# Kernel tuning notes

Hardware: AMD Instinct MI355X
Metric: run time of the kernel (lower is better)

The kernel has to match this reference:

```python
import jax, jax.numpy as jnp
import numpy as np

B, N, T = 64, 256, 512          # batch, num_objs, num_triples
DO, DP, H, DOUT = 512, 512, 512, 512


def setup_inputs() -> dict:
    key = jax.random.key(0)
    ks = jax.random.split(key, 12)

    def kaiming(k, shape):
        fan_in = shape[0]
        return jax.random.normal(k, shape, jnp.float32) * np.sqrt(2.0 / fan_in)

    return {
        "obj_vecs": jax.random.normal(ks[0], (B, N, DO), jnp.float32),
        "pred_vecs": jax.random.normal(ks[1], (B, T, DP), jnp.float32),
        "edges": jax.random.randint(ks[2], (B, T, 3), 0, N, jnp.int64),
        # net1: [2*DO+DP -> H -> 2*H+DOUT], ReLU after each Linear
        "n1_w1": kaiming(ks[3], (2 * DO + DP, H)),
        "n1_b1": jnp.zeros((H,), jnp.float32),
        "n1_w2": kaiming(ks[4], (H, 2 * H + DOUT)),
        "n1_b2": jnp.zeros((2 * H + DOUT,), jnp.float32),
        # net2: [H -> H -> DOUT], ReLU after each Linear
        "n2_w1": kaiming(ks[5], (H, H)),
        "n2_b1": jnp.zeros((H,), jnp.float32),
        "n2_w2": kaiming(ks[6], (H, DOUT)),
        "n2_b2": jnp.zeros((DOUT,), jnp.float32),
    }


def reference(obj_vecs, pred_vecs, edges,
              n1_w1, n1_b1, n1_w2, n1_b2,
              n2_w1, n2_b1, n2_w2, n2_b2):
    num_batch, num_objs, _ = obj_vecs.shape
    h_dim = n1_b1.shape[0]
    d_out = n2_w2.shape[1]

    s_idx = edges[:, :, 0]            # [B, T] subject node ids
    o_idx = edges[:, :, 2]            # [B, T] object node ids

    # gather subject/object vectors per triple
    cur_s = jnp.take_along_axis(obj_vecs, s_idx[:, :, None], axis=1)  # [B,T,DO]
    cur_o = jnp.take_along_axis(obj_vecs, o_idx[:, :, None], axis=1)  # [B,T,DO]
    cur_t = jnp.concatenate([cur_s, pred_vecs, cur_o], axis=-1)       # [B,T,2DO+DP]

    # net1 MLP (Linear+ReLU, Linear+ReLU)
    hid = jax.nn.relu(jnp.einsum('btd,dh->bth', cur_t, n1_w1) + n1_b1)
    new_t = jax.nn.relu(jnp.einsum('bth,hk->btk', hid, n1_w2) + n1_b2)

    new_s = new_t[:, :, :h_dim]
    new_p = new_t[:, :, h_dim:h_dim + d_out]
    new_o = new_t[:, :, h_dim + d_out:2 * h_dim + d_out]

    # scatter-add back to nodes, per batch element
    b_ix = jnp.arange(num_batch)[:, None]            # [B,1]
    pooled = jnp.zeros((num_batch, num_objs, h_dim), obj_vecs.dtype)
    pooled = pooled.at[b_ix, s_idx].add(new_s)
    pooled = pooled.at[b_ix, o_idx].add(new_o)

    # avg pooling: divide by per-node incidence count (clamped at 1)
    ones = jnp.ones(s_idx.shape, obj_vecs.dtype)
    counts = jnp.zeros((num_batch, num_objs), obj_vecs.dtype)
    counts = counts.at[b_ix, s_idx].add(ones)
    counts = counts.at[b_ix, o_idx].add(ones)
    counts = jnp.maximum(counts, 1.0)
    pooled = pooled / counts[:, :, None]

    # net2 MLP (Linear+ReLU, Linear+ReLU)
    h2 = jax.nn.relu(jnp.einsum('bnh,hk->bnk', pooled, n2_w1) + n2_b1)
    new_obj_vecs = jax.nn.relu(jnp.einsum('bnh,hd->bnd', h2, n2_w2) + n2_b2)

    return new_obj_vecs, new_p
```

## Files before the change

### kernel.cpp

```cpp
#include <hip/hip_runtime.h>

typedef __bf16 bf16;
typedef __attribute__((ext_vector_type(2))) __bf16 bf16x2;
typedef __attribute__((ext_vector_type(4))) __bf16 bf16x4;
typedef __attribute__((ext_vector_type(8))) __bf16 bf16x8;
typedef __attribute__((ext_vector_type(4))) float f32x4;

#define DEVINL __device__ __forceinline__

typedef __attribute__((address_space(1))) void gvoid_t;
typedef __attribute__((address_space(3))) void lvoid_t;

DEVINL void async_ld16(const void* g, void* l) {
    __builtin_amdgcn_global_load_lds((gvoid_t*)g, (lvoid_t*)l, 16, 0, 0);
}

template<int MODE, int NBN>
__global__ __launch_bounds__(256, 2) void gemm_k(
    const bf16* __restrict__ A, const bf16* __restrict__ Bt,
    const float* __restrict__ bias, bf16* __restrict__ Dbf,
    float* __restrict__ Df, bf16* __restrict__ Dbf2,
    const int* __restrict__ edges, const bf16* __restrict__ obj,
    const bf16* __restrict__ pred, int K)
{
    const int tid = threadIdx.x;
    const int id = blockIdx.x;
    const int bn = (id >> 3) % NBN;
    const int bm = (id & 7) + 8 * ((id >> 3) / NBN);

    __shared__ __align__(16) bf16 lds[2 * 128 * 64];
    bf16* ldsA = lds;
    bf16* ldsB = lds + 128 * 64;

    const int g_slot = tid & 7;
    const int row0 = tid >> 3;

    unsigned offS[4], offP[4], offO[4], offA[4], offB[4];
#pragma unroll
    for (int i = 0; i < 4; i++) {
        int r = row0 + 32 * i;
        int gr = bm * 128 + r;
        if (MODE == 0) {
            int b = gr >> 9;
            int s = edges[gr * 3 + 0] & 255;
            int o = edges[gr * 3 + 2] & 255;
            offS[i] = (unsigned)(b * 256 + s) * 512u;
            offP[i] = (unsigned)gr * 512u;
            offO[i] = (unsigned)(b * 256 + o) * 512u;
        } else {
            offA[i] = (unsigned)gr * (unsigned)K;
        }
        offB[i] = (unsigned)(bn * 128 + r) * (unsigned)K;
    }

    f32x4 acc[4][4];
    const f32x4 zero4 = {0.f, 0.f, 0.f, 0.f};
#pragma unroll
    for (int i = 0; i < 4; i++)
#pragma unroll
        for (int j = 0; j < 4; j++) acc[i][j] = zero4;

    const int wave = tid >> 6;
    const int lane = tid & 63;
    const int wr = (wave >> 1) * 64;
    const int wc = (wave & 1) * 64;
    const int lq = lane >> 4;
    const int lr = lane & 15;

    const int KT = K >> 6;
    for (int kt = 0; kt < KT; ++kt) {
        __syncthreads();
#pragma unroll
        for (int i = 0; i < 4; i++) {
            int r = row0 + 32 * i;
            int gsrc = g_slot ^ (r & 7);
            const bf16* gp;
            if (MODE == 0) {
                int region = kt >> 3;
                unsigned col = (unsigned)((kt & 7) * 64 + gsrc * 8);
                if (region == 0)      gp = obj + offS[i] + col;
                else if (region == 1) gp = pred + offP[i] + col;
                else                  gp = obj + offO[i] + col;
            } else {
                gp = A + offA[i] + (unsigned)(kt * 64 + gsrc * 8);
            }
            async_ld16(gp, ldsA + (tid + i * 256) * 8);
        }
#pragma unroll
        for (int i = 0; i < 4; i++) {
            int r = row0 + 32 * i;
            int gsrc = g_slot ^ (r & 7);
            async_ld16(Bt + offB[i] + (unsigned)(kt * 64 + gsrc * 8),
                       ldsB + (tid + i * 256) * 8);
        }
        __syncthreads();

#pragma unroll
        for (int ks = 0; ks < 2; ++ks) {
            bf16x8 af[4], bfr[4];
#pragma unroll
            for (int mi = 0; mi < 4; ++mi) {
                int r = wr + mi * 16 + lr;
                int g = (ks * 4 + lq) ^ (r & 7);
                af[mi] = *(const bf16x8*)(ldsA + (r * 8 + g) * 8);
            }
#pragma unroll
            for (int ni = 0; ni < 4; ++ni) {
                int r = wc + ni * 16 + lr;
                int g = (ks * 4 + lq) ^ (r & 7);
                bfr[ni] = *(const bf16x8*)(ldsB + (r * 8 + g) * 8);
            }
#pragma unroll
            for (int mi = 0; mi < 4; ++mi)
#pragma unroll
                for (int ni = 0; ni < 4; ++ni)
                    acc[mi][ni] = __builtin_amdgcn_mfma_f32_16x16x32_bf16(
                        bfr[ni], af[mi], acc[mi][ni], 0, 0, 0);
        }
    }

    __syncthreads();

    const int rb = bm * 128 + wr;
    const bool f32path = (MODE == 3) || (MODE == 1 && bn >= 4 && bn < 8);

    if (!f32path) {
        bf16* cw = lds + wave * 4096;
        const bf16*  dummy = nullptr; (void)dummy;
        bf16* outp;
        int cb;
        if (MODE == 1) {
            if (bn < 4) { outp = Dbf;  cb = bn * 128 + wc; }
            else        { outp = Dbf2; cb = bn * 128 + wc - 1024; }
        } else {
            outp = Dbf; cb = bn * 128 + wc;
        }
#pragma unroll
        for (int ni = 0; ni < 4; ++ni) {
            const f32x4 bv = *(const f32x4*)(bias + bn * 128 + wc + ni * 16 + lq * 4);
#pragma unroll
            for (int mi = 0; mi < 4; ++mi) {
                f32x4 v = acc[mi][ni];
                int row = mi * 16 + lr;
                int sl = (ni * 2 + (lq >> 1)) ^ (row & 7);
                bf16x4 o4;
#pragma unroll
                for (int r = 0; r < 4; r++) {
                    float t = v[r] + bv[r];
                    o4[r] = (bf16)(t > 0.f ? t : 0.f);
                }
                *(bf16x4*)(cw + row * 64 + sl * 8 + (lq & 1) * 4) = o4;
            }
        }
#pragma unroll
        for (int it = 0; it < 8; ++it) {
            int g = it * 64 + lane;
            int row = g >> 3, k = g & 7;
            bf16x8 v = *(const bf16x8*)(cw + row * 64 + ((k ^ (row & 7)) * 8));
            *(bf16x8*)(outp + (unsigned)(rb + row) * 512u + cb + k * 8) = v;
        }
    } else {
        float* cwf = (float*)lds + wave * 2048;
        const int cbf = (MODE == 1) ? (bn * 128 + wc - 512) : (bn * 128 + wc);
#pragma unroll
        for (int half = 0; half < 2; ++half) {
#pragma unroll
            for (int ni = 0; ni < 4; ++ni) {
                const f32x4 bv = *(const f32x4*)(bias + bn * 128 + wc + ni * 16 + lq * 4);
#pragma unroll
                for (int mi2 = 0; mi2 < 2; ++mi2) {
                    f32x4 v = acc[half * 2 + mi2][ni];
                    int row = mi2 * 16 + lr;
                    int s16 = ni * 4 + lq;
                    int sl = (s16 & 8) | ((s16 & 7) ^ (row & 7));
                    f32x4 x;
#pragma unroll
                    for (int r = 0; r < 4; r++) {
                        float t = v[r] + bv[r];
                        x[r] = t > 0.f ? t : 0.f;
                    }
                    *(f32x4*)(cwf + row * 64 + sl * 4) = x;
                }
            }
#pragma unroll
            for (int it = 0; it < 8; ++it) {
                int g = it * 64 + lane;
                int row = g >> 4, k = g & 15;
                int kk = (k & 8) | ((k & 7) ^ (row & 7));
                f32x4 v = *(const f32x4*)(cwf + row * 64 + kk * 4);
                *(f32x4*)(Df + (unsigned)(rb + half * 32 + row) * 512u + cbf + k * 4) = v;
            }
        }
    }
}

__global__ void pre_k(const float4* __restrict__ o, const float4* __restrict__ p,
                      bf16x4* __restrict__ ob, bf16x4* __restrict__ pb,
                      const float* __restrict__ w1, bf16* __restrict__ w1t,
                      const float* __restrict__ w2, bf16* __restrict__ w2t,
                      const float* __restrict__ w3, bf16* __restrict__ w3t,
                      const float* __restrict__ w4, bf16* __restrict__ w4t) {
    __shared__ float tile[32][33];
    int blk = blockIdx.x;
    int t = threadIdx.x;
    if (blk >= 24576) {
        int id = blk - 24576;
        const float* src; bf16* dst; int R, C, bx, by;
        if (id < 768)       { src = w1; dst = w1t; R = 1536; C = 512;  bx = id % 16; by = id / 16; }
        else if (id < 1536) { id -= 768;  src = w2; dst = w2t; R = 512; C = 1536; bx = id % 48; by = id / 48; }
        else if (id < 1792) { id -= 1536; src = w3; dst = w3t; R = 512; C = 512;  bx = id % 16; by = id / 16; }
        else                { id -= 1792; src = w4; dst = w4t; R = 512; C = 512;  bx = id % 16; by = id / 16; }
        int c0 = bx * 32, r0 = by * 32;
        int tx = t & 31, ty = t >> 5;
#pragma unroll
        for (int i = 0; i < 4; i++)
            tile[ty + i * 8][tx] = src[(size_t)(r0 + ty + i * 8) * C + c0 + tx];
        __syncthreads();
#pragma unroll
        for (int i = 0; i < 4; i++)
            dst[(size_t)(c0 + ty + i * 8) * R + r0 + tx] = (bf16)tile[tx][ty + i * 8];
        return;
    }
    int i = blk * 256 + t;
    if (i < 2097152) {
        float4 v = o[i];
        bf16x4 r = { (bf16)v.x, (bf16)v.y, (bf16)v.z, (bf16)v.w };
        ob[i] = r;
    } else {
        int j = i - 2097152;
        float4 v = p[j];
        bf16x4 r = { (bf16)v.x, (bf16)v.y, (bf16)v.z, (bf16)v.w };
        pb[j] = r;
    }
}

__global__ __launch_bounds__(256) void pool3_k(
    const int* __restrict__ edges,
    const bf16* __restrict__ new_s, const bf16* __restrict__ new_o,
    bf16* __restrict__ out)
{
    __shared__ int ent[1024];
    __shared__ int ec;
    const int idx = blockIdx.x;
    const int b = idx >> 8, n = idx & 255;
    const int t = threadIdx.x;
    if (t == 0) ec = 0;
    __syncthreads();
#pragma unroll
    for (int e0 = 0; e0 < 2; e0++) {
        int row = b * 512 + t + e0 * 256;
        int s = edges[row * 3 + 0] & 255;
        int o = edges[row * 3 + 2] & 255;
        if (s == n) { int ps = atomicAdd(&ec, 1); ent[ps] = row << 1; }
        if (o == n) { int po = atomicAdd(&ec, 1); ent[po] = (row << 1) | 1; }
    }
    __syncthreads();
    const int c = ec;
    float a0 = 0.f, a1 = 0.f;
    for (int j = 0; j < c; ++j) {
        int v = ent[j];
        const bf16x2* rp = (const bf16x2*)(((v & 1) ? new_o : new_s) +
                                           (unsigned)(v >> 1) * 512u);
        bf16x2 w = rp[t];
        a0 += (float)w[0];
        a1 += (float)w[1];
    }
    float inv = 1.f / (float)(c > 1 ? c : 1);
    bf16x2 o2 = { (bf16)(a0 * inv), (bf16)(a1 * inv) };
    *(bf16x2*)(out + (unsigned)idx * 512u + (unsigned)(t * 2)) = o2;
}

extern "C" void kernel_launch(void* const* d_in, const int* in_sizes, int n_in,
                              void* d_out, int out_size, void* d_ws, size_t ws_size,
                              hipStream_t stream) {
    const float* obj_f  = (const float*)d_in[0];
    const float* pred_f = (const float*)d_in[1];
    const int*   edges  = (const int*)d_in[2];
    const float* w1 = (const float*)d_in[3];
    const float* b1 = (const float*)d_in[4];
    const float* w2 = (const float*)d_in[5];
    const float* b2 = (const float*)d_in[6];
    const float* w3 = (const float*)d_in[7];
    const float* b3 = (const float*)d_in[8];
    const float* w4 = (const float*)d_in[9];
    const float* b4 = (const float*)d_in[10];

    char* ws = (char*)d_ws;
    bf16* obj_bf  = (bf16*)(ws + 0);
    bf16* pred_bf = (bf16*)(ws + 16777216);
    bf16* new_s   = (bf16*)(ws + 0);
    bf16* w1t = (bf16*)(ws + 50331648);
    bf16* w2t = (bf16*)(ws + 51904512);
    bf16* w3t = (bf16*)(ws + 53477376);
    bf16* w4t = (bf16*)(ws + 54001664);
    bf16* hid = (bf16*)(ws + 54525952);
    bf16* pooled_bf = hid;
    bf16* h2  = (bf16*)(ws + 71303168);

    float* out_obj = (float*)d_out;
    float* out_p   = (float*)d_out + 8388608;
    bf16* new_o    = (bf16*)d_out;

    pre_k<<<26624, 256, 0, stream>>>((const float4*)obj_f, (const float4*)pred_f,
                                     (bf16x4*)obj_bf, (bf16x4*)pred_bf,
                                     w1, w1t, w2, w2t, w3, w3t, w4, w4t);

    gemm_k<0, 4><<<1024, 256, 0, stream>>>(
        nullptr, w1t, b1, hid, nullptr, nullptr, edges, obj_bf, pred_bf, 1536);

    gemm_k<1, 12><<<3072, 256, 0, stream>>>(
        hid, w2t, b2, new_s, out_p, new_o, nullptr, nullptr, nullptr, 512);

    pool3_k<<<16384, 256, 0, stream>>>(edges, new_s, new_o, pooled_bf);

    gemm_k<2, 4><<<512, 256, 0, stream>>>(
        pooled_bf, w3t, b3, h2, nullptr, nullptr, nullptr, nullptr, nullptr, 512);

    gemm_k<3, 4><<<512, 256, 0, stream>>>(
        h2, w4t, b4, nullptr, out_obj, nullptr, nullptr, nullptr, nullptr, 512);
}
```

Measured before the change: 367.0 us.

## Use 256x256-tile 8-wave pipelined GEMM kernel for net1 layers

Adds a new 512-thread GEMM kernel with 256x256 output tiles, double-buffered LDS staging in quarter chunks, and explicit vmcnt/lgkmcnt waits so global-to-LDS loads and register fragment loads overlap MFMA work. The two large net1 GEMMs (gather-fused first layer and the wide second layer) move to it, while net2 keeps the old 128x128 kernel, now trimmed to its two modes. The larger tiles raise arithmetic intensity and cut redundant operand loads. In exchange they use 128 KB of LDS, many accumulator registers and fewer blocks, which could limit occupancy and tail balance.

```diff
diff --git a/kernel.cpp b/kernel.cpp
--- a/kernel.cpp
+++ b/kernel.cpp
@@ -15,41 +15,250 @@
     __builtin_amdgcn_global_load_lds((gvoid_t*)g, (lvoid_t*)l, 16, 0, 0);
 }
 
-template<int MODE, int NBN>
-__global__ __launch_bounds__(256, 2) void gemm_k(
+DEVINL void wait_vm6()   { asm volatile("s_waitcnt vmcnt(6)" ::: "memory"); }
+DEVINL void wait_vm4()   { asm volatile("s_waitcnt vmcnt(4)" ::: "memory"); }
+DEVINL void wait_vm0()   { asm volatile("s_waitcnt vmcnt(0)" ::: "memory"); }
+DEVINL void wait_lgkm0() { asm volatile("s_waitcnt lgkmcnt(0)" ::: "memory");
+                           __builtin_amdgcn_sched_barrier(0); }
+DEVINL void barrier_()   { __builtin_amdgcn_s_barrier();
+                           __builtin_amdgcn_sched_barrier(0); }
+
+template<int MODE>
+__global__ __launch_bounds__(512, 2) void gemm8_k(
     const bf16* __restrict__ A, const bf16* __restrict__ Bt,
     const float* __restrict__ bias, bf16* __restrict__ Dbf,
     float* __restrict__ Df, bf16* __restrict__ Dbf2,
     const int* __restrict__ edges, const bf16* __restrict__ obj,
-    const bf16* __restrict__ pred, int K)
+    const bf16* __restrict__ pred, int K, int NBN)
 {
     const int tid = threadIdx.x;
     const int id = blockIdx.x;
     const int bn = (id >> 3) % NBN;
     const int bm = (id & 7) + 8 * ((id >> 3) / NBN);
 
-    __shared__ __align__(16) bf16 lds[2 * 128 * 64];
-    bf16* ldsA = lds;
-    bf16* ldsB = lds + 128 * 64;
+    __shared__ __align__(16) bf16 lds[8 * 8192];
 
     const int g_slot = tid & 7;
     const int row0 = tid >> 3;
 
     unsigned offS[4], offP[4], offO[4], offA[4], offB[4];
 #pragma unroll
-    for (int i = 0; i < 4; i++) {
-        int r = row0 + 32 * i;
-        int gr = bm * 128 + r;
+    for (int hi = 0; hi < 4; hi++) {
+        int r = (hi >> 1) * 128 + (hi & 1) * 64 + row0;
+        int gr = bm * 256 + r;
         if (MODE == 0) {
             int b = gr >> 9;
             int s = edges[gr * 3 + 0] & 255;
             int o = edges[gr * 3 + 2] & 255;
-            offS[i] = (unsigned)(b * 256 + s) * 512u;
-            offP[i] = (unsigned)gr * 512u;
-            offO[i] = (unsigned)(b * 256 + o) * 512u;
+            offS[hi] = (unsigned)(b * 256 + s) * 512u;
+            offP[hi] = (unsigned)gr * 512u;
+            offO[hi] = (unsigned)(b * 256 + o) * 512u;
         } else {
-            offA[i] = (unsigned)gr * (unsigned)K;
-        }
+            offA[hi] = (unsigned)gr * (unsigned)K;
+        }
+        offB[hi] = (unsigned)(bn * 256 + r) * (unsigned)K;
+    }
+
+    auto STAGE = [&](int tt, int kind) {
+        bf16* ldst = lds + ((tt & 1) * 4 + kind) * 8192;
+        int h = kind & 1;
+#pragma unroll
+        for (int i = 0; i < 2; i++) {
+            int r = i * 64 + row0;
+            int gsrc = g_slot ^ (r & 7);
+            int hi = h * 2 + i;
+            const bf16* gp;
+            if (kind < 2) {
+                if (MODE == 0) {
+                    int region = tt >> 3;
+                    unsigned col = (unsigned)((tt & 7) * 64 + gsrc * 8);
+                    if (region == 0)      gp = obj + offS[hi] + col;
+                    else if (region == 1) gp = pred + offP[hi] + col;
+                    else                  gp = obj + offO[hi] + col;
+                } else {
+                    gp = A + offA[hi] + (unsigned)(tt * 64 + gsrc * 8);
+                }
+            } else {
+                gp = Bt + offB[hi] + (unsigned)(tt * 64 + gsrc * 8);
+            }
+            async_ld16(gp, ldst + (tid + i * 512) * 8);
+        }
+    };
+
+    f32x4 acc[8][4];
+    const f32x4 zero4 = {0.f, 0.f, 0.f, 0.f};
+#pragma unroll
+    for (int i = 0; i < 8; i++)
+#pragma unroll
+        for (int j = 0; j < 4; j++) acc[i][j] = zero4;
+
+    const int wave = tid >> 6, lane = tid & 63;
+    const int wm = wave >> 2, wn = wave & 3;
+    const int lq = lane >> 4, lr = lane & 15;
+
+    bf16x8 af0[8], af1[8], b0r[4], b1r[4];
+
+    auto LDA = [&](int tt, int ks, bf16x8* d) {
+        const bf16* base = lds + ((tt & 1) * 4 + wm) * 8192;
+#pragma unroll
+        for (int mi = 0; mi < 8; mi++) {
+            int rr = mi * 16 + lr;
+            int g = (ks * 4 + lq) ^ (rr & 7);
+            d[mi] = *(const bf16x8*)(base + (rr * 8 + g) * 8);
+        }
+    };
+    auto LDB = [&](int tt, int ks, bf16x8* d) {
+        const bf16* base = lds + ((tt & 1) * 4 + 2 + (wn >> 1)) * 8192;
+#pragma unroll
+        for (int ni = 0; ni < 4; ni++) {
+            int rr = (wn & 1) * 64 + ni * 16 + lr;
+            int g = (ks * 4 + lq) ^ (rr & 7);
+            d[ni] = *(const bf16x8*)(base + (rr * 8 + g) * 8);
+        }
+    };
+    auto MM = [&](const bf16x8* a, const bf16x8* b, int mh) {
+        __builtin_amdgcn_s_setprio(1);
+#pragma unroll
+        for (int mi = 0; mi < 4; mi++)
+#pragma unroll
+            for (int ni = 0; ni < 4; ni++)
+                acc[mh * 4 + mi][ni] = __builtin_amdgcn_mfma_f32_16x16x32_bf16(
+                    b[ni], a[mh * 4 + mi], acc[mh * 4 + mi][ni], 0, 0, 0);
+        __builtin_amdgcn_s_setprio(0);
+        __builtin_amdgcn_sched_barrier(0);
+    };
+
+    STAGE(0, 0); STAGE(0, 1); STAGE(0, 2); STAGE(0, 3);
+
+    const int NT = K >> 6;
+    for (int t = 0; ; ++t) {
+        if (t < NT) {
+            if (t + 1 < NT) { STAGE(t + 1, 0); wait_vm6(); }
+            else            wait_vm4();
+        } else wait_vm0();
+        barrier_();
+        if (t < NT) LDA(t, 0, af0);
+        wait_lgkm0();
+        if (t >= 1) MM(af1, b1r, 0);
+        barrier_();
+        if (t < NT) {
+            if (t + 1 < NT) { STAGE(t + 1, 1); wait_vm4(); }
+            else            wait_vm0();
+        }
+        barrier_();
+        if (t < NT) LDB(t, 0, b0r);
+        wait_lgkm0();
+        if (t >= 1) MM(af1, b1r, 1);
+        barrier_();
+        if (t == NT) break;
+        if (t + 1 < NT) STAGE(t + 1, 2);
+        barrier_();
+        LDA(t, 1, af1);
+        wait_lgkm0();
+        MM(af0, b0r, 0);
+        barrier_();
+        if (t + 1 < NT) STAGE(t + 1, 3);
+        barrier_();
+        LDB(t, 1, b1r);
+        wait_lgkm0();
+        MM(af0, b0r, 1);
+        barrier_();
+    }
+
+    const int rowbase = bm * 256 + wm * 128;
+    const int cb0 = bn * 256 + wn * 64;
+    const bool f32p = (MODE == 1) && (cb0 >= 512) && (cb0 < 1024);
+
+    if (!f32p) {
+        bf16* cw = lds + wave * 8192;
+        bf16* outp; int cb;
+        if (MODE == 1) {
+            if (cb0 < 512) { outp = Dbf;  cb = cb0; }
+            else           { outp = Dbf2; cb = cb0 - 1024; }
+        } else { outp = Dbf; cb = cb0; }
+#pragma unroll
+        for (int ni = 0; ni < 4; ++ni) {
+            const f32x4 bv = *(const f32x4*)(bias + cb0 + ni * 16 + lq * 4);
+#pragma unroll
+            for (int mi = 0; mi < 8; ++mi) {
+                f32x4 v = acc[mi][ni];
+                int row = mi * 16 + lr;
+                int sl = (ni * 2 + (lq >> 1)) ^ (row & 7);
+                bf16x4 o4;
+#pragma unroll
+                for (int r = 0; r < 4; r++) {
+                    float x = v[r] + bv[r];
+                    o4[r] = (bf16)(x > 0.f ? x : 0.f);
+                }
+                *(bf16x4*)(cw + row * 64 + sl * 8 + (lq & 1) * 4) = o4;
+            }
+        }
+#pragma unroll
+        for (int it = 0; it < 16; ++it) {
+            int g = it * 64 + lane;
+            int row = g >> 3, k = g & 7;
+            bf16x8 v = *(const bf16x8*)(cw + row * 64 + ((k ^ (row & 7)) * 8));
+            *(bf16x8*)(outp + (unsigned)(rowbase + row) * 512u + cb + k * 8) = v;
+        }
+    } else {
+        float* cwf = (float*)lds + wave * 4096;
+        const int cbf = cb0 - 512;
+#pragma unroll
+        for (int mh = 0; mh < 2; ++mh) {
+#pragma unroll
+            for (int ni = 0; ni < 4; ++ni) {
+                const f32x4 bv = *(const f32x4*)(bias + cb0 + ni * 16 + lq * 4);
+#pragma unroll
+                for (int mi2 = 0; mi2 < 4; ++mi2) {
+                    f32x4 v = acc[mh * 4 + mi2][ni];
+                    int row = mi2 * 16 + lr;
+                    int s16 = ni * 4 + lq;
+                    int sl = (s16 & 8) | ((s16 & 7) ^ (row & 7));
+                    f32x4 x;
+#pragma unroll
+                    for (int r = 0; r < 4; r++) {
+                        float tt = v[r] + bv[r];
+                        x[r] = tt > 0.f ? tt : 0.f;
+                    }
+                    *(f32x4*)(cwf + row * 64 + sl * 4) = x;
+                }
+            }
+#pragma unroll
+            for (int it = 0; it < 16; ++it) {
+                int g = it * 64 + lane;
+                int row = g >> 4, k = g & 15;
+                int kk = (k & 8) | ((k & 7) ^ (row & 7));
+                f32x4 v = *(const f32x4*)(cwf + row * 64 + kk * 4);
+                *(f32x4*)(Df + (unsigned)(rowbase + mh * 64 + row) * 512u
+                          + cbf + k * 4) = v;
+            }
+        }
+    }
+}
+
+template<int MODE, int NBN>
+__global__ __launch_bounds__(256, 2) void gemm_k(
+    const bf16* __restrict__ A, const bf16* __restrict__ Bt,
+    const float* __restrict__ bias, bf16* __restrict__ Dbf,
+    float* __restrict__ Df, int K)
+{
+    const int tid = threadIdx.x;
+    const int id = blockIdx.x;
+    const int bn = (id >> 3) % NBN;
+    const int bm = (id & 7) + 8 * ((id >> 3) / NBN);
+
+    __shared__ __align__(16) bf16 lds[2 * 128 * 64];
+    bf16* ldsA = lds;
+    bf16* ldsB = lds + 128 * 64;
+
+    const int g_slot = tid & 7;
+    const int row0 = tid >> 3;
+
+    unsigned offA[4], offB[4];
+#pragma unroll
+    for (int i = 0; i < 4; i++) {
+        int r = row0 + 32 * i;
+        offA[i] = (unsigned)(bm * 128 + r) * (unsigned)K;
         offB[i] = (unsigned)(bn * 128 + r) * (unsigned)K;
     }
 
@@ -74,17 +283,8 @@
         for (int i = 0; i < 4; i++) {
             int r = row0 + 32 * i;
             int gsrc = g_slot ^ (r & 7);
-            const bf16* gp;
-            if (MODE == 0) {
-                int region = kt >> 3;
-                unsigned col = (unsigned)((kt & 7) * 64 + gsrc * 8);
-                if (region == 0)      gp = obj + offS[i] + col;
-                else if (region == 1) gp = pred + offP[i] + col;
-                else                  gp = obj + offO[i] + col;
-            } else {
-                gp = A + offA[i] + (unsigned)(kt * 64 + gsrc * 8);
-            }
-            async_ld16(gp, ldsA + (tid + i * 256) * 8);
+            async_ld16(A + offA[i] + (unsigned)(kt * 64 + gsrc * 8),
+                       ldsA + (tid + i * 256) * 8);
         }
 #pragma unroll
         for (int i = 0; i < 4; i++) {
@@ -120,24 +320,14 @@
     }
 
     __syncthreads();
-
     const int rb = bm * 128 + wr;
-    const bool f32path = (MODE == 3) || (MODE == 1 && bn >= 4 && bn < 8);
-
-    if (!f32path) {
+
+    if (MODE == 2) {
         bf16* cw = lds + wave * 4096;
-        const bf16*  dummy = nullptr; (void)dummy;
-        bf16* outp;
-        int cb;
-        if (MODE == 1) {
-            if (bn < 4) { outp = Dbf;  cb = bn * 128 + wc; }
-            else        { outp = Dbf2; cb = bn * 128 + wc - 1024; }
-        } else {
-            outp = Dbf; cb = bn * 128 + wc;
-        }
+        const int cb = bn * 128 + wc;
 #pragma unroll
         for (int ni = 0; ni < 4; ++ni) {
-            const f32x4 bv = *(const f32x4*)(bias + bn * 128 + wc + ni * 16 + lq * 4);
+            const f32x4 bv = *(const f32x4*)(bias + cb + ni * 16 + lq * 4);
 #pragma unroll
             for (int mi = 0; mi < 4; ++mi) {
                 f32x4 v = acc[mi][ni];
@@ -157,16 +347,16 @@
             int g = it * 64 + lane;
             int row = g >> 3, k = g & 7;
             bf16x8 v = *(const bf16x8*)(cw + row * 64 + ((k ^ (row & 7)) * 8));
-            *(bf16x8*)(outp + (unsigned)(rb + row) * 512u + cb + k * 8) = v;
+            *(bf16x8*)(Dbf + (unsigned)(rb + row) * 512u + cb + k * 8) = v;
         }
     } else {
         float* cwf = (float*)lds + wave * 2048;
-        const int cbf = (MODE == 1) ? (bn * 128 + wc - 512) : (bn * 128 + wc);
+        const int cbf = bn * 128 + wc;
 #pragma unroll
         for (int half = 0; half < 2; ++half) {
 #pragma unroll
             for (int ni = 0; ni < 4; ++ni) {
-                const f32x4 bv = *(const f32x4*)(bias + bn * 128 + wc + ni * 16 + lq * 4);
+                const f32x4 bv = *(const f32x4*)(bias + cbf + ni * 16 + lq * 4);
 #pragma unroll
                 for (int mi2 = 0; mi2 < 2; ++mi2) {
                     f32x4 v = acc[half * 2 + mi2][ni];
@@ -305,17 +495,17 @@
                                      (bf16x4*)obj_bf, (bf16x4*)pred_bf,
                                      w1, w1t, w2, w2t, w3, w3t, w4, w4t);
 
-    gemm_k<0, 4><<<1024, 256, 0, stream>>>(
-        nullptr, w1t, b1, hid, nullptr, nullptr, edges, obj_bf, pred_bf, 1536);
-
-    gemm_k<1, 12><<<3072, 256, 0, stream>>>(
-        hid, w2t, b2, new_s, out_p, new_o, nullptr, nullptr, nullptr, 512);
+    gemm8_k<0><<<256, 512, 0, stream>>>(
+        nullptr, w1t, b1, hid, nullptr, nullptr, edges, obj_bf, pred_bf,
+        1536, 2);
+
+    gemm8_k<1><<<768, 512, 0, stream>>>(
+        hid, w2t, b2, new_s, out_p, new_o, nullptr, nullptr, nullptr,
+        512, 6);
 
     pool3_k<<<16384, 256, 0, stream>>>(edges, new_s, new_o, pooled_bf);
 
-    gemm_k<2, 4><<<512, 256, 0, stream>>>(
-        pooled_bf, w3t, b3, h2, nullptr, nullptr, nullptr, nullptr, nullptr, 512);
-
-    gemm_k<3, 4><<<512, 256, 0, stream>>>(
-        h2, w4t, b4, nullptr, out_obj, nullptr, nullptr, nullptr, nullptr, 512);
+    gemm_k<2, 4><<<512, 256, 0, stream>>>(pooled_bf, w3t, b3, h2, nullptr, 512);
+
+    gemm_k<3, 4><<<512, 256, 0, stream>>>(h2, w4t, b4, nullptr, out_obj, 512);
 }
```

New measurement: 1.126 ms. +206.7%, slower.
